# Kernel tuning notes

Hardware: AMD Instinct MI355X
Metric: run time of the kernel (lower is better)

## Reference

```python
import jax, jax.numpy as jnp
import numpy as np

B, L, E, H, K = 256, 500, 300, 10, 5  # batch, doc_len, word_embedding, h1, num_aspects


def setup_inputs() -> dict:
    key = jax.random.key(0)
    k1, k2, k3 = jax.random.split(key, 3)
    review = jax.random.normal(k1, (B, L, E), dtype=jnp.float32)
    # params initialized uniform(-0.01, 0.01) as in the torch module
    aspProj = jax.random.uniform(k2, (K, E, H), dtype=jnp.float32, minval=-0.01, maxval=0.01)
    aspEmbed = jax.random.uniform(k3, (K, 3 * H), dtype=jnp.float32, minval=-0.01, maxval=0.01)
    return {"review": review, "aspProj": aspProj, "aspEmbed": aspEmbed}


def reference(review, aspProj, aspEmbed):
    # project review into each aspect subspace: (K, B, L, H)
    proj = jnp.einsum('ble,keh->kblh', review, aspProj)
    # pad seq dim by 1 on each side, build window-3 unfold.
    # torch unfold(1,3,1) yields (B, L, H, 3) then reshape to (B, L, 3*H),
    # i.e. feature layout is (h_index, window_offset) -- match by stacking
    # window offsets on the LAST axis before the reshape.
    padded = jnp.pad(proj, ((0, 0), (0, 0), (1, 1), (0, 0)))
    windows = jnp.stack([padded[:, :, i:i + L, :] for i in range(3)], axis=-1)  # (K,B,L,H,3)
    windows = windows.reshape(K, windows.shape[1], L, 3 * H)  # (K,B,L,3H)
    # attention logits per position, softmax over the WHOLE sequence dim
    scores = jnp.einsum('kblf,kf->kbl', windows, aspEmbed)
    attn = jax.nn.softmax(scores, axis=-1)  # (K,B,L)
    # attention-weighted sum over sequence -> aspect representation
    rep = jnp.einsum('kblh,kbl->kbh', proj, attn)  # (K,B,H)
    batch_aspAttn = jnp.transpose(attn, (1, 0, 2))  # (B,K,L)
    batch_aspRep = jnp.transpose(rep, (1, 0, 2))    # (B,K,H)
    return (batch_aspAttn, batch_aspRep)
```

## Files before the change

### kernel.cpp

```cpp
#include <hip/hip_runtime.h>

#define BB 256
#define LL 500
#define EE 300
#define HH 10
#define KK 5
#define NF 50
#define NWAVE 8

#define BP 328
#define AP 72
#define PW 52
#define MPB 512
#define NR4 75

#define WS_BT_BYTES  (64 * BP * 2)
#define WS_PROJ_OFF  65536

typedef __attribute__((ext_vector_type(8))) short short8;
typedef __attribute__((ext_vector_type(4))) float f32x4;

__device__ __forceinline__ unsigned int f2bf(float x) {
    unsigned int u = __float_as_uint(x);
    return (u + 0x7FFFu + ((u >> 16) & 1u)) >> 16;
}

__global__ void k0_bt(const float* __restrict__ aspProj, short* __restrict__ btw) {
    int j = blockIdx.x * 512 + threadIdx.x;
    if (j >= 64 * BP) return;
    int n = j / BP, e = j - n * BP;
    float v = 0.f;
    if (n < NF && e < EE) v = aspProj[(n / HH) * (EE * HH) + e * HH + (n - (n / HH) * HH)];
    btw[j] = (short)f2bf(v);
}

__global__ __launch_bounds__(512, 4) void k1_gemm(
    const float* __restrict__ review,
    const short* __restrict__ btw,
    float* __restrict__ projw)
{
    __shared__ short sB[64 * BP];
    __shared__ short sA[2][128 * AP];

    const int tid  = threadIdx.x;
    const int b    = blockIdx.x >> 2;
    const int rq   = blockIdx.x & 3;
    const int lane = tid & 63;
    const int w    = tid >> 6;
    const int quad = lane >> 4;
    const int m16  = lane & 15;
    const int q    = tid & 15;
    const int r0   = tid >> 4;

    {
        const int4* src = (const int4*)btw;
        int4* dst = (int4*)sB;
        for (int j = tid; j < WS_BT_BYTES / 16; j += 512) dst[j] = src[j];
    }

    const float4* rev4 = (const float4*)review + (size_t)b * LL * NR4;
    const float4* rp[4];
#pragma unroll
    for (int i = 0; i < 4; ++i) {
        int r = rq * 128 + r0 + 32 * i;
        rp[i] = rev4 + (size_t)((r < LL) ? r : (LL - 1)) * NR4;
    }

    float4 ld[4];
#pragma unroll
    for (int i = 0; i < 4; ++i) ld[i] = rp[i][q];

#pragma unroll
    for (int i = 0; i < 4; ++i) {
        int r = r0 + 32 * i;
        uint2 pk;
        pk.x = f2bf(ld[i].x) | (f2bf(ld[i].y) << 16);
        pk.y = f2bf(ld[i].z) | (f2bf(ld[i].w) << 16);
        *(uint2*)&sA[0][r * AP + q * 4] = pk;
    }
    __syncthreads();

    f32x4 acc[4];
#pragma unroll
    for (int ni = 0; ni < 4; ++ni) acc[ni] = (f32x4){0.f, 0.f, 0.f, 0.f};

#pragma unroll
    for (int c = 0; c < 5; ++c) {
        if (c + 1 < 5) {
            int fq = (c + 1) * 16 + q;
            if (fq > NR4 - 1) fq = NR4 - 1;
#pragma unroll
            for (int i = 0; i < 4; ++i) ld[i] = rp[i][fq];
        }
        const short* Ac = sA[c & 1];
#pragma unroll
        for (int s = 0; s < 2; ++s) {
            short8 af = *(const short8*)&Ac[(w * 16 + m16) * AP + s * 32 + quad * 8];
            short8 bf[4];
#pragma unroll
            for (int ni = 0; ni < 4; ++ni)
                bf[ni] = *(const short8*)&sB[(ni * 16 + m16) * BP + c * 64 + s * 32 + quad * 8];
#pragma unroll
            for (int ni = 0; ni < 4; ++ni)
                acc[ni] = __builtin_amdgcn_mfma_f32_16x16x32_bf16(af, bf[ni], acc[ni], 0, 0, 0);
        }
        if (c + 1 < 5) {
            short* An = sA[(c + 1) & 1];
#pragma unroll
            for (int i = 0; i < 4; ++i) {
                int r = r0 + 32 * i;
                uint2 pk;
                pk.x = f2bf(ld[i].x) | (f2bf(ld[i].y) << 16);
                pk.y = f2bf(ld[i].z) | (f2bf(ld[i].w) << 16);
                *(uint2*)&An[r * AP + q * 4] = pk;
            }
            __syncthreads();
        }
    }

    float* pw = projw + (size_t)b * MPB * PW;
    const int rowbase = rq * 128 + w * 16 + quad * 4;
#pragma unroll
    for (int ni = 0; ni < 4; ++ni) {
        int col = ni * 16 + m16;
        if (col < NF) {
#pragma unroll
            for (int r = 0; r < 4; ++r)
                pw[(size_t)(rowbase + r) * PW + col] = acc[ni][r];
        }
    }
}

__global__ __launch_bounds__(512, 2) void k2_attn(
    const float* __restrict__ projw,
    const float* __restrict__ aspEmbed,
    float* __restrict__ out)
{
    __shared__ float s_d[3 * KK * MPB];
    __shared__ float s_red[KK * NWAVE];
    __shared__ float s_rep[NWAVE * NF];
    __shared__ float s_emb[KK * 3 * HH];

    const int tid  = threadIdx.x;
    const int b    = blockIdx.x;
    const int lane = tid & 63;
    const int w    = tid >> 6;
    const int l    = tid;
    const bool vl  = (l < LL);

    if (tid < KK * 3 * HH) s_emb[tid] = aspEmbed[tid];

    float4 prv[13];
    const float4* pr4 = (const float4*)(projw + (size_t)b * MPB * PW + (size_t)l * PW);
#pragma unroll
    for (int i = 0; i < 13; ++i) prv[i] = pr4[i];
    float pr[52];
#pragma unroll
    for (int i = 0; i < 13; ++i) {
        pr[4 * i + 0] = prv[i].x; pr[4 * i + 1] = prv[i].y;
        pr[4 * i + 2] = prv[i].z; pr[4 * i + 3] = prv[i].w;
    }
    __syncthreads();

    float d0[KK], d1[KK], d2[KK];
#pragma unroll
    for (int k = 0; k < KK; ++k) {
        float a0 = 0.f, a1 = 0.f, a2 = 0.f;
#pragma unroll
        for (int h = 0; h < HH; ++h) {
            float x = pr[k * HH + h];
            a0 = fmaf(x, s_emb[k * 3 * HH + 3 * h + 0], a0);
            a1 = fmaf(x, s_emb[k * 3 * HH + 3 * h + 1], a1);
            a2 = fmaf(x, s_emb[k * 3 * HH + 3 * h + 2], a2);
        }
        d0[k] = vl ? a0 : 0.f;
        d1[k] = vl ? a1 : 0.f;
        d2[k] = vl ? a2 : 0.f;
    }
#pragma unroll
    for (int k = 0; k < KK; ++k) {
        s_d[(0 * KK + k) * MPB + l] = d0[k];
        s_d[(1 * KK + k) * MPB + l] = d1[k];
        s_d[(2 * KK + k) * MPB + l] = d2[k];
    }
    __syncthreads();

    const int lp1 = (l + 1 < MPB) ? l + 1 : MPB - 1;
    float sc[KK];
#pragma unroll
    for (int k = 0; k < KK; ++k) {
        float t0 = (l >= 1) ? s_d[(0 * KK + k) * MPB + l - 1] : 0.f;
        float t1 = s_d[(1 * KK + k) * MPB + l];
        float t2 = s_d[(2 * KK + k) * MPB + lp1];
        sc[k] = vl ? (t0 + t1 + t2) : -1e30f;
    }

    float mx[KK];
#pragma unroll
    for (int k = 0; k < KK; ++k) {
        float m = sc[k];
        for (int s = 32; s > 0; s >>= 1) m = fmaxf(m, __shfl_xor(m, s, 64));
        if (lane == 0) s_red[k * NWAVE + w] = m;
    }
    __syncthreads();
#pragma unroll
    for (int k = 0; k < KK; ++k) {
        float m = s_red[k * NWAVE + 0];
#pragma unroll
        for (int ww = 1; ww < NWAVE; ++ww) m = fmaxf(m, s_red[k * NWAVE + ww]);
        mx[k] = m;
    }
    __syncthreads();
    float ex[KK], sm[KK];
#pragma unroll
    for (int k = 0; k < KK; ++k) {
        ex[k] = __expf(sc[k] - mx[k]);
        float s = ex[k];
        for (int sh = 32; sh > 0; sh >>= 1) s += __shfl_xor(s, sh, 64);
        if (lane == 0) s_red[k * NWAVE + w] = s;
    }
    __syncthreads();
#pragma unroll
    for (int k = 0; k < KK; ++k) {
        float s = 0.f;
#pragma unroll
        for (int ww = 0; ww < NWAVE; ++ww) s += s_red[k * NWAVE + ww];
        sm[k] = s;
    }

#pragma unroll
    for (int k = 0; k < KK; ++k) {
        float wk = ex[k] / sm[k];
        if (vl) out[((size_t)b * KK + k) * LL + l] = wk;
#pragma unroll
        for (int h = 0; h < HH; ++h) {
            float v = pr[k * HH + h] * wk;
            for (int sh = 32; sh > 0; sh >>= 1) v += __shfl_xor(v, sh, 64);
            if (lane == 0) s_rep[w * NF + k * HH + h] = v;
        }
    }
    __syncthreads();
    if (tid < NF) {
        float s = 0.f;
#pragma unroll
        for (int ww = 0; ww < NWAVE; ++ww) s += s_rep[ww * NF + tid];
        out[(size_t)BB * KK * LL + (size_t)b * NF + tid] = s;
    }
}

extern "C" void kernel_launch(void* const* d_in, const int* in_sizes, int n_in,
                              void* d_out, int out_size, void* d_ws, size_t ws_size,
                              hipStream_t stream) {
    const float* review   = (const float*)d_in[0];
    const float* aspProj  = (const float*)d_in[1];
    const float* aspEmbed = (const float*)d_in[2];
    float* out   = (float*)d_out;
    short* btw   = (short*)d_ws;
    float* projw = (float*)((char*)d_ws + WS_PROJ_OFF);

    k0_bt  <<<dim3((64 * BP + 511) / 512), dim3(512), 0, stream>>>(aspProj, btw);
    k1_gemm<<<dim3(BB * 4), dim3(512), 0, stream>>>(review, btw, projw);
    k2_attn<<<dim3(BB), dim3(512), 0, stream>>>(projw, aspEmbed, out);
}
```

Baseline: 252.2 us.

## Load GEMM A-fragments directly from global memory, dropping shared staging

The GEMM kernel no longer stages review rows through a double-buffered shared-memory tile. Each lane now loads its own float4 pairs straight from global memory, converts them to bf16 in registers, and feeds the MFMA directly. Blocks shrink to 256 threads covering 64 rows each, so twice as many blocks are launched. This removes the LDS writes and per-chunk barriers, at the cost of more scattered global access per lane, less latency hiding from prefetch, and re-copying the B tile into shared memory in twice as many blocks.

```diff
diff --git a/kernel.cpp b/kernel.cpp
--- a/kernel.cpp
+++ b/kernel.cpp
@@ -9,7 +9,6 @@
 #define NWAVE 8
 
 #define BP 328
-#define AP 72
 #define PW 52
 #define MPB 512
 #define NR4 75
@@ -34,50 +33,31 @@
     btw[j] = (short)f2bf(v);
 }
 
-__global__ __launch_bounds__(512, 4) void k1_gemm(
+__global__ __launch_bounds__(256, 3) void k1_gemm(
     const float* __restrict__ review,
     const short* __restrict__ btw,
     float* __restrict__ projw)
 {
     __shared__ short sB[64 * BP];
-    __shared__ short sA[2][128 * AP];
 
     const int tid  = threadIdx.x;
-    const int b    = blockIdx.x >> 2;
-    const int rq   = blockIdx.x & 3;
+    const int b    = blockIdx.x >> 3;
+    const int rg   = blockIdx.x & 7;
     const int lane = tid & 63;
     const int w    = tid >> 6;
     const int quad = lane >> 4;
     const int m16  = lane & 15;
-    const int q    = tid & 15;
-    const int r0   = tid >> 4;
 
     {
         const int4* src = (const int4*)btw;
         int4* dst = (int4*)sB;
-        for (int j = tid; j < WS_BT_BYTES / 16; j += 512) dst[j] = src[j];
-    }
-
-    const float4* rev4 = (const float4*)review + (size_t)b * LL * NR4;
-    const float4* rp[4];
-#pragma unroll
-    for (int i = 0; i < 4; ++i) {
-        int r = rq * 128 + r0 + 32 * i;
-        rp[i] = rev4 + (size_t)((r < LL) ? r : (LL - 1)) * NR4;
-    }
-
-    float4 ld[4];
-#pragma unroll
-    for (int i = 0; i < 4; ++i) ld[i] = rp[i][q];
-
-#pragma unroll
-    for (int i = 0; i < 4; ++i) {
-        int r = r0 + 32 * i;
-        uint2 pk;
-        pk.x = f2bf(ld[i].x) | (f2bf(ld[i].y) << 16);
-        pk.y = f2bf(ld[i].z) | (f2bf(ld[i].w) << 16);
-        *(uint2*)&sA[0][r * AP + q * 4] = pk;
-    }
+        for (int j = tid; j < WS_BT_BYTES / 16; j += 256) dst[j] = src[j];
+    }
+
+    const int row = rg * 64 + w * 16 + m16;
+    const int rc  = (row < LL) ? row : (LL - 1);
+    const float4* rp = (const float4*)review + (size_t)b * LL * NR4 + (size_t)rc * NR4;
+
     __syncthreads();
 
     f32x4 acc[4];
@@ -85,41 +65,29 @@
     for (int ni = 0; ni < 4; ++ni) acc[ni] = (f32x4){0.f, 0.f, 0.f, 0.f};
 
 #pragma unroll
-    for (int c = 0; c < 5; ++c) {
-        if (c + 1 < 5) {
-            int fq = (c + 1) * 16 + q;
-            if (fq > NR4 - 1) fq = NR4 - 1;
-#pragma unroll
-            for (int i = 0; i < 4; ++i) ld[i] = rp[i][fq];
-        }
-        const short* Ac = sA[c & 1];
-#pragma unroll
-        for (int s = 0; s < 2; ++s) {
-            short8 af = *(const short8*)&Ac[(w * 16 + m16) * AP + s * 32 + quad * 8];
-            short8 bf[4];
-#pragma unroll
-            for (int ni = 0; ni < 4; ++ni)
-                bf[ni] = *(const short8*)&sB[(ni * 16 + m16) * BP + c * 64 + s * 32 + quad * 8];
-#pragma unroll
-            for (int ni = 0; ni < 4; ++ni)
-                acc[ni] = __builtin_amdgcn_mfma_f32_16x16x32_bf16(af, bf[ni], acc[ni], 0, 0, 0);
-        }
-        if (c + 1 < 5) {
-            short* An = sA[(c + 1) & 1];
-#pragma unroll
-            for (int i = 0; i < 4; ++i) {
-                int r = r0 + 32 * i;
-                uint2 pk;
-                pk.x = f2bf(ld[i].x) | (f2bf(ld[i].y) << 16);
-                pk.y = f2bf(ld[i].z) | (f2bf(ld[i].w) << 16);
-                *(uint2*)&An[r * AP + q * 4] = pk;
-            }
-            __syncthreads();
-        }
+    for (int c = 0; c < 10; ++c) {
+        int e4 = c * 8 + quad * 2;
+        int e4a = (e4     < NR4) ? e4     : (NR4 - 1);
+        int e4b = (e4 + 1 < NR4) ? e4 + 1 : (NR4 - 1);
+        float4 va = rp[e4a];
+        float4 vb = rp[e4b];
+        short8 af;
+        af[0] = (short)f2bf(va.x); af[1] = (short)f2bf(va.y);
+        af[2] = (short)f2bf(va.z); af[3] = (short)f2bf(va.w);
+        af[4] = (short)f2bf(vb.x); af[5] = (short)f2bf(vb.y);
+        af[6] = (short)f2bf(vb.z); af[7] = (short)f2bf(vb.w);
+
+        short8 bf[4];
+#pragma unroll
+        for (int ni = 0; ni < 4; ++ni)
+            bf[ni] = *(const short8*)&sB[(ni * 16 + m16) * BP + c * 32 + quad * 8];
+#pragma unroll
+        for (int ni = 0; ni < 4; ++ni)
+            acc[ni] = __builtin_amdgcn_mfma_f32_16x16x32_bf16(af, bf[ni], acc[ni], 0, 0, 0);
     }
 
     float* pw = projw + (size_t)b * MPB * PW;
-    const int rowbase = rq * 128 + w * 16 + quad * 4;
+    const int rowbase = rg * 64 + w * 16 + quad * 4;
 #pragma unroll
     for (int ni = 0; ni < 4; ++ni) {
         int col = ni * 16 + m16;
@@ -259,6 +227,6 @@
     float* projw = (float*)((char*)d_ws + WS_PROJ_OFF);
 
     k0_bt  <<<dim3((64 * BP + 511) / 512), dim3(512), 0, stream>>>(aspProj, btw);
-    k1_gemm<<<dim3(BB * 4), dim3(512), 0, stream>>>(review, btw, projw);
+    k1_gemm<<<dim3(BB * 8), dim3(256), 0, stream>>>(review, btw, projw);
     k2_attn<<<dim3(BB), dim3(512), 0, stream>>>(projw, aspEmbed, out);
 }
```

Measured after the change: 254.3 us. About the same (+0.8%).
